# Kernel optimization log

Measured on AMD Instinct MI355X. Metric: run time of the kernel, lower is better.

## Reference

```python
import jax, jax.numpy as jnp
import numpy as np

B, L, D = 8, 30, 512
NS, NI = 21, 8  # n_slot_caps = n_slots+1, n_intent_caps = n_intents+1


def setup_inputs() -> dict:
    key = jax.random.key(0)
    ks = jax.random.split(key, 6)
    s = 0.02  # keep pose magnitudes sane
    return {
        "token_features": jax.random.normal(ks[0], (B, L, D), jnp.float32),
        "cls_token": jax.random.normal(ks[1], (B, D), jnp.float32),
        "w_route_ws": jax.random.normal(ks[2], (L, NS, D), jnp.float32) * s,
        "w_pose_ws": jax.random.normal(ks[3], (L, NS, D, D), jnp.float32) * s,
        "w_route_si": jax.random.normal(ks[4], (NS, NI, D), jnp.float32) * s,
        "w_pose_si": jax.random.normal(ks[5], (NS, NI, D, D), jnp.float32) * s,
    }


def reference(token_features, cls_token, w_route_ws, w_pose_ws, w_route_si, w_pose_si):
    d_model = token_features.shape[-1]
    # ---- route words -> slots ----
    a_words = token_features.sum(-1) / d_model                      # (b, l)
    c_ws = jax.nn.softmax(
        jnp.einsum('lnj,blj->bln', w_route_ws, token_features), axis=-1)  # (b, l, n_slot)
    wc = c_ws * a_words[:, :, None]                                 # (b, l, n_slot)
    weighted_c = wc.sum(axis=1)                                     # (b, n_slot)
    a_slots = weighted_c / a_words.sum(-1, keepdims=True)           # (b, n_slot)
    u_hat_slots = jnp.einsum('lnij,blj->blni', w_pose_ws, token_features)  # (b, l, n_slot, d)
    u_slots = jnp.einsum('bls,blsk->bsk', wc, u_hat_slots) / weighted_c[:, :, None]
    slots = jnp.argmax(c_ws, axis=-1)                               # (b, l)
    # ---- route slots -> intents ----
    c_si = jax.nn.softmax(
        jnp.einsum('sij,bsj->bsi', w_route_si, u_slots), axis=-1)   # (b, n_slot, n_int)
    wc2 = c_si * a_slots[:, :, None]                                # (b, n_slot, n_int)
    weighted_c2 = wc2.sum(axis=1)                                   # (b, n_int)
    a_intents = weighted_c2 / a_slots.sum(-1, keepdims=True)        # (b, n_int)
    u_hat_intents = jnp.einsum('sijk,bsk->bsik', w_pose_si, u_slots)  # (b, n_slot, n_int, d)
    u_intents = jnp.einsum('bsi,bsik->bik', wc2, u_hat_intents) / weighted_c2[:, :, None]
    # ---- argmax dispatch + cls residual ----
    max_idx = jnp.argmax(a_intents, axis=-1)                        # (b,)
    poses = jnp.take_along_axis(u_intents, max_idx[:, None, None], axis=1)[:, 0, :]
    intents = cls_token + poses                                     # (b, d)
    return (slots, intents)
```

## Files before the change

### kernel.cpp

```cpp
#include <hip/hip_runtime.h>

#define B 8
#define L 30
#define D 512
#define NS 21
#define NI 8

__device__ __forceinline__ float block_reduce_sum_256(float v, float* red) {
  int lane = threadIdx.x & 63;
  int wid  = threadIdx.x >> 6;
  #pragma unroll
  for (int o = 32; o > 0; o >>= 1) v += __shfl_down(v, o, 64);
  __syncthreads();
  if (lane == 0) red[wid] = v;
  __syncthreads();
  float r = 0.f;
  if (threadIdx.x == 0) {
    #pragma unroll
    for (int w = 0; w < 4; w++) r += red[w];
  }
  return r;
}

__global__ void k_phase_a(const float* __restrict__ x,
                          const float* __restrict__ w_route_ws,
                          float* __restrict__ wc,
                          float* __restrict__ a_words,
                          float* __restrict__ slots_out) {
  __shared__ float red[4];
  __shared__ float logits[NS];
  __shared__ float s_aw;
  int bl = blockIdx.x;
  int l  = bl % L;
  const float* xv = x + (size_t)bl * D;

  float p = 0.f;
  for (int j = threadIdx.x; j < D; j += 256) p += xv[j];
  float tot = block_reduce_sum_256(p, red);
  if (threadIdx.x == 0) { s_aw = tot / (float)D; a_words[bl] = s_aw; }

  for (int n = 0; n < NS; n++) {
    const float* wr = w_route_ws + (size_t)(l * NS + n) * D;
    float q = 0.f;
    for (int j = threadIdx.x; j < D; j += 256) q += wr[j] * xv[j];
    float t = block_reduce_sum_256(q, red);
    if (threadIdx.x == 0) logits[n] = t;
  }
  __syncthreads();
  if (threadIdx.x == 0) {
    float m = logits[0]; int am = 0;
    #pragma unroll
    for (int n = 1; n < NS; n++) if (logits[n] > m) { m = logits[n]; am = n; }
    float e[NS]; float se = 0.f;
    #pragma unroll
    for (int n = 0; n < NS; n++) { e[n] = __expf(logits[n] - m); se += e[n]; }
    float sc = s_aw / se;
    #pragma unroll
    for (int n = 0; n < NS; n++) wc[(size_t)bl * NS + n] = e[n] * sc;
    slots_out[bl] = (float)am;
  }
}

__global__ void k_stats1(const float* __restrict__ wc,
                         const float* __restrict__ a_words,
                         float* __restrict__ weighted_c,
                         float* __restrict__ a_slots) {
  __shared__ float aw_sum[B];
  int t = threadIdx.x;
  if (t < B) {
    float s = 0.f;
    for (int l = 0; l < L; l++) s += a_words[t * L + l];
    aw_sum[t] = s;
  }
  __syncthreads();
  if (t < B * NS) {
    int b = t / NS, n = t % NS;
    float s = 0.f;
    for (int l = 0; l < L; l++) s += wc[(size_t)(b * L + l) * NS + n];
    weighted_c[t] = s;
    a_slots[t] = s / aw_sum[b];
  }
}

__global__ void __launch_bounds__(256) k_u_slots(
    const float* __restrict__ x,
    const float* __restrict__ w_pose_ws,
    const float* __restrict__ wc,
    const float* __restrict__ weighted_c,
    float* __restrict__ u_slots) {
  __shared__ float lwc[B * L];
  __shared__ float lwcn[B];
  int n     = blockIdx.x >> 5;
  int itile = blockIdx.x & 31;
  int wave  = threadIdx.x >> 6;
  int lane  = threadIdx.x & 63;
  int i0    = itile * 16 + wave * 4;

  if (threadIdx.x < B * L) lwc[threadIdx.x] = wc[(size_t)threadIdx.x * NS + n];
  if (threadIdx.x >= 240 && threadIdx.x < 240 + B)
    lwcn[threadIdx.x - 240] = weighted_c[(threadIdx.x - 240) * NS + n];
  __syncthreads();

  float acc[4][B];
  #pragma unroll
  for (int r = 0; r < 4; r++)
    #pragma unroll
    for (int b = 0; b < B; b++) acc[r][b] = 0.f;

  for (int l = 0; l < L; l++) {
    const float* wrow = w_pose_ws + ((size_t)(l * NS + n) * D + i0) * D;
    float4 w0[4], w1[4];
    #pragma unroll
    for (int r = 0; r < 4; r++) {
      const float4* wp = (const float4*)(wrow + (size_t)r * D) + lane * 2;
      w0[r] = wp[0]; w1[r] = wp[1];
    }
    #pragma unroll
    for (int b = 0; b < B; b++) {
      const float4* xp = (const float4*)(x + (size_t)(b * L + l) * D) + lane * 2;
      float4 x0 = xp[0], x1 = xp[1];
      float wcl = lwc[b * L + l];
      #pragma unroll
      for (int r = 0; r < 4; r++) {
        float t = w0[r].x * x0.x + w0[r].y * x0.y + w0[r].z * x0.z + w0[r].w * x0.w
                + w1[r].x * x1.x + w1[r].y * x1.y + w1[r].z * x1.z + w1[r].w * x1.w;
        acc[r][b] += wcl * t;
      }
    }
  }
  #pragma unroll
  for (int r = 0; r < 4; r++)
    #pragma unroll
    for (int b = 0; b < B; b++)
      #pragma unroll
      for (int o = 32; o > 0; o >>= 1) acc[r][b] += __shfl_xor(acc[r][b], o, 64);
  if (lane == 0) {
    #pragma unroll
    for (int r = 0; r < 4; r++)
      #pragma unroll
      for (int b = 0; b < B; b++)
        u_slots[((size_t)b * NS + n) * D + (i0 + r)] = acc[r][b] / lwcn[b];
  }
}

__global__ void k_route_si(const float* __restrict__ u_slots,
                           const float* __restrict__ w_route_si,
                           const float* __restrict__ a_slots,
                           float* __restrict__ wc2) {
  __shared__ float red[4];
  __shared__ float logits[NI];
  int bs = blockIdx.x;
  int s  = bs % NS;
  const float* uv = u_slots + (size_t)bs * D;
  for (int i = 0; i < NI; i++) {
    const float* wr = w_route_si + (size_t)(s * NI + i) * D;
    float q = 0.f;
    for (int j = threadIdx.x; j < D; j += 256) q += wr[j] * uv[j];
    float t = block_reduce_sum_256(q, red);
    if (threadIdx.x == 0) logits[i] = t;
  }
  __syncthreads();
  if (threadIdx.x == 0) {
    float m = logits[0];
    #pragma unroll
    for (int i = 1; i < NI; i++) m = fmaxf(m, logits[i]);
    float e[NI]; float se = 0.f;
    #pragma unroll
    for (int i = 0; i < NI; i++) { e[i] = __expf(logits[i] - m); se += e[i]; }
    float sc = a_slots[bs] / se;
    #pragma unroll
    for (int i = 0; i < NI; i++) wc2[(size_t)bs * NI + i] = e[i] * sc;
  }
}

__global__ void k_stats2(const float* __restrict__ wc2,
                         const float* __restrict__ a_slots,
                         float* __restrict__ weighted_c2,
                         int* __restrict__ max_idx) {
  __shared__ float asum[B];
  __shared__ float ai[B * NI];
  int t = threadIdx.x;
  if (t < B) {
    float s = 0.f;
    for (int n = 0; n < NS; n++) s += a_slots[t * NS + n];
    asum[t] = s;
  }
  float w = 0.f;
  if (t < B * NI) {
    int b = t / NI, i = t % NI;
    for (int ss = 0; ss < NS; ss++) w += wc2[(size_t)(b * NS + ss) * NI + i];
    weighted_c2[t] = w;
  }
  __syncthreads();
  if (t < B * NI) ai[t] = w / asum[t / NI];
  __syncthreads();
  if (t < B) {
    float m = ai[t * NI]; int am = 0;
    #pragma unroll
    for (int i = 1; i < NI; i++) { float v = ai[t * NI + i]; if (v > m) { m = v; am = i; } }
    max_idx[t] = am;
  }
}

__global__ void k_pose_si(const float* __restrict__ w_pose_si,
                          const float* __restrict__ u_slots,
                          const float* __restrict__ wc2,
                          const int* __restrict__ max_idx,
                          float* __restrict__ poses) {
  const int JS = 4;
  int idx = blockIdx.x;
  int b   = idx / (NS * JS);
  int rem = idx - b * (NS * JS);
  int s   = rem / JS, jc = rem % JS;
  int i   = max_idx[b];
  int k   = threadIdx.x;
  const float* wb = w_pose_si + (size_t)(s * NI + i) * D * D + k;
  float cs = 0.f;
  int j0 = jc * (D / JS);
  #pragma unroll 8
  for (int j = j0; j < j0 + D / JS; j++) cs += wb[(size_t)j * D];
  float val = wc2[(size_t)(b * NS + s) * NI + i] *
              u_slots[(size_t)(b * NS + s) * D + k] * cs;
  atomicAdd(&poses[b * D + k], val);
}

__global__ void k_final(const float* __restrict__ cls,
                        const float* __restrict__ poses,
                        const float* __restrict__ weighted_c2,
                        const int* __restrict__ max_idx,
                        float* __restrict__ out_intents) {
  int b = blockIdx.x, k = threadIdx.x;
  out_intents[b * D + k] =
      cls[b * D + k] + poses[b * D + k] / weighted_c2[b * NI + max_idx[b]];
}

extern "C" void kernel_launch(void* const* d_in, const int* in_sizes, int n_in,
                              void* d_out, int out_size, void* d_ws, size_t ws_size,
                              hipStream_t stream) {
  const float* x    = (const float*)d_in[0];
  const float* cls  = (const float*)d_in[1];
  const float* wrws = (const float*)d_in[2];
  const float* wpws = (const float*)d_in[3];
  const float* wrsi = (const float*)d_in[4];
  const float* wpsi = (const float*)d_in[5];

  float* out         = (float*)d_out;
  float* slots_out   = out;
  float* intents_out = out + B * L;

  float* wsf         = (float*)d_ws;
  float* wc          = wsf;
  float* a_words     = wc + B * L * NS;
  float* weighted_c  = a_words + B * L;
  float* a_slots     = weighted_c + B * NS;
  float* u_slots     = a_slots + B * NS;
  float* wc2         = u_slots + B * NS * D;
  float* weighted_c2 = wc2 + B * NS * NI;
  float* poses       = weighted_c2 + B * NI;
  int*   max_idx     = (int*)(poses + B * D);

  hipMemsetAsync(poses, 0, B * D * sizeof(float), stream);
  k_phase_a<<<B * L, 256, 0, stream>>>(x, wrws, wc, a_words, slots_out);
  k_stats1<<<1, 256, 0, stream>>>(wc, a_words, weighted_c, a_slots);
  k_u_slots<<<NS * 32, 256, 0, stream>>>(x, wpws, wc, weighted_c, u_slots);
  k_route_si<<<B * NS, 256, 0, stream>>>(u_slots, wrsi, a_slots, wc2);
  k_stats2<<<1, 256, 0, stream>>>(wc2, a_slots, weighted_c2, max_idx);
  k_pose_si<<<B * NS * 4, 512, 0, stream>>>(wpsi, u_slots, wc2, max_idx, poses);
  k_final<<<B, 512, 0, stream>>>(cls, poses, weighted_c2, max_idx, intents_out);
}
```

Baseline: 1.036 ms.

## Split u_slots over L chunks, dedupe pose_si column sums, wave-level routing dots

```diff
diff --git a/kernel.cpp b/kernel.cpp
--- a/kernel.cpp
+++ b/kernel.cpp
@@ -5,48 +5,44 @@
 #define D 512
 #define NS 21
 #define NI 8
-
-__device__ __forceinline__ float block_reduce_sum_256(float v, float* red) {
+#define LC 5
+#define LPC (L / LC)
+
+__global__ void __launch_bounds__(256) k_phase_a(
+    const float* __restrict__ x,
+    const float* __restrict__ w_route_ws,
+    float* __restrict__ wc,
+    float* __restrict__ a_words,
+    float* __restrict__ slots_out) {
+  __shared__ float logits[NS];
+  int bl   = blockIdx.x;
+  int l    = bl % L;
+  int wave = threadIdx.x >> 6;
   int lane = threadIdx.x & 63;
-  int wid  = threadIdx.x >> 6;
-  #pragma unroll
-  for (int o = 32; o > 0; o >>= 1) v += __shfl_down(v, o, 64);
-  __syncthreads();
-  if (lane == 0) red[wid] = v;
-  __syncthreads();
-  float r = 0.f;
-  if (threadIdx.x == 0) {
-    #pragma unroll
-    for (int w = 0; w < 4; w++) r += red[w];
-  }
-  return r;
-}
-
-__global__ void k_phase_a(const float* __restrict__ x,
-                          const float* __restrict__ w_route_ws,
-                          float* __restrict__ wc,
-                          float* __restrict__ a_words,
-                          float* __restrict__ slots_out) {
-  __shared__ float red[4];
-  __shared__ float logits[NS];
-  __shared__ float s_aw;
-  int bl = blockIdx.x;
-  int l  = bl % L;
-  const float* xv = x + (size_t)bl * D;
-
-  float p = 0.f;
-  for (int j = threadIdx.x; j < D; j += 256) p += xv[j];
-  float tot = block_reduce_sum_256(p, red);
-  if (threadIdx.x == 0) { s_aw = tot / (float)D; a_words[bl] = s_aw; }
-
-  for (int n = 0; n < NS; n++) {
-    const float* wr = w_route_ws + (size_t)(l * NS + n) * D;
-    float q = 0.f;
-    for (int j = threadIdx.x; j < D; j += 256) q += wr[j] * xv[j];
-    float t = block_reduce_sum_256(q, red);
-    if (threadIdx.x == 0) logits[n] = t;
-  }
-  __syncthreads();
+
+  const float4* xp = (const float4*)(x + (size_t)bl * D) + lane * 2;
+  float4 x0 = xp[0], x1 = xp[1];
+
+  float aw = 0.f;
+  if (wave == 0) {
+    float s = x0.x + x0.y + x0.z + x0.w + x1.x + x1.y + x1.z + x1.w;
+    #pragma unroll
+    for (int o = 32; o > 0; o >>= 1) s += __shfl_xor(s, o, 64);
+    aw = s / (float)D;
+    if (lane == 0) a_words[bl] = aw;
+  }
+
+  for (int n = wave; n < NS; n += 4) {
+    const float4* wp = (const float4*)(w_route_ws + (size_t)(l * NS + n) * D) + lane * 2;
+    float4 w0 = wp[0], w1 = wp[1];
+    float q = w0.x * x0.x + w0.y * x0.y + w0.z * x0.z + w0.w * x0.w
+            + w1.x * x1.x + w1.y * x1.y + w1.z * x1.z + w1.w * x1.w;
+    #pragma unroll
+    for (int o = 32; o > 0; o >>= 1) q += __shfl_xor(q, o, 64);
+    if (lane == 0) logits[n] = q;
+  }
+  __syncthreads();
+
   if (threadIdx.x == 0) {
     float m = logits[0]; int am = 0;
     #pragma unroll
@@ -54,7 +50,7 @@
     float e[NS]; float se = 0.f;
     #pragma unroll
     for (int n = 0; n < NS; n++) { e[n] = __expf(logits[n] - m); se += e[n]; }
-    float sc = s_aw / se;
+    float sc = aw / se;
     #pragma unroll
     for (int n = 0; n < NS; n++) wc[(size_t)bl * NS + n] = e[n] * sc;
     slots_out[bl] = (float)am;
@@ -86,19 +82,18 @@
     const float* __restrict__ x,
     const float* __restrict__ w_pose_ws,
     const float* __restrict__ wc,
-    const float* __restrict__ weighted_c,
-    float* __restrict__ u_slots) {
+    float* __restrict__ u_part) {
   __shared__ float lwc[B * L];
-  __shared__ float lwcn[B];
-  int n     = blockIdx.x >> 5;
-  int itile = blockIdx.x & 31;
+  int bid   = blockIdx.x;
+  int n     = bid / (32 * LC);
+  int rem   = bid % (32 * LC);
+  int itile = rem / LC;
+  int lc    = rem % LC;
   int wave  = threadIdx.x >> 6;
   int lane  = threadIdx.x & 63;
   int i0    = itile * 16 + wave * 4;
 
   if (threadIdx.x < B * L) lwc[threadIdx.x] = wc[(size_t)threadIdx.x * NS + n];
-  if (threadIdx.x >= 240 && threadIdx.x < 240 + B)
-    lwcn[threadIdx.x - 240] = weighted_c[(threadIdx.x - 240) * NS + n];
   __syncthreads();
 
   float acc[4][B];
@@ -107,7 +102,8 @@
     #pragma unroll
     for (int b = 0; b < B; b++) acc[r][b] = 0.f;
 
-  for (int l = 0; l < L; l++) {
+  int l0 = lc * LPC;
+  for (int l = l0; l < l0 + LPC; l++) {
     const float* wrow = w_pose_ws + ((size_t)(l * NS + n) * D + i0) * D;
     float4 w0[4], w1[4];
     #pragma unroll
@@ -139,25 +135,47 @@
     for (int r = 0; r < 4; r++)
       #pragma unroll
       for (int b = 0; b < B; b++)
-        u_slots[((size_t)b * NS + n) * D + (i0 + r)] = acc[r][b] / lwcn[b];
-  }
-}
-
-__global__ void k_route_si(const float* __restrict__ u_slots,
-                           const float* __restrict__ w_route_si,
-                           const float* __restrict__ a_slots,
-                           float* __restrict__ wc2) {
-  __shared__ float red[4];
+        u_part[(((size_t)lc * B + b) * NS + n) * D + (i0 + r)] = acc[r][b];
+  }
+}
+
+__global__ void k_div_u(const float* __restrict__ u_part,
+                        const float* __restrict__ weighted_c,
+                        float* __restrict__ u_slots) {
+  int bn = blockIdx.x;
+  int b  = bn / NS, n = bn % NS;
+  float wcn = weighted_c[bn];
+  for (int k = threadIdx.x; k < D; k += 256) {
+    float s = 0.f;
+    #pragma unroll
+    for (int lc = 0; lc < LC; lc++)
+      s += u_part[(((size_t)lc * B + b) * NS + n) * D + k];
+    u_slots[(size_t)bn * D + k] = s / wcn;
+  }
+}
+
+__global__ void __launch_bounds__(256) k_route_si(
+    const float* __restrict__ u_slots,
+    const float* __restrict__ w_route_si,
+    const float* __restrict__ a_slots,
+    float* __restrict__ wc2) {
   __shared__ float logits[NI];
-  int bs = blockIdx.x;
-  int s  = bs % NS;
-  const float* uv = u_slots + (size_t)bs * D;
-  for (int i = 0; i < NI; i++) {
-    const float* wr = w_route_si + (size_t)(s * NI + i) * D;
-    float q = 0.f;
-    for (int j = threadIdx.x; j < D; j += 256) q += wr[j] * uv[j];
-    float t = block_reduce_sum_256(q, red);
-    if (threadIdx.x == 0) logits[i] = t;
+  int bs   = blockIdx.x;
+  int s    = bs % NS;
+  int wave = threadIdx.x >> 6;
+  int lane = threadIdx.x & 63;
+
+  const float4* up = (const float4*)(u_slots + (size_t)bs * D) + lane * 2;
+  float4 u0 = up[0], u1 = up[1];
+
+  for (int i = wave; i < NI; i += 4) {
+    const float4* wp = (const float4*)(w_route_si + (size_t)(s * NI + i) * D) + lane * 2;
+    float4 w0 = wp[0], w1 = wp[1];
+    float q = w0.x * u0.x + w0.y * u0.y + w0.z * u0.z + w0.w * u0.w
+            + w1.x * u1.x + w1.y * u1.y + w1.z * u1.z + w1.w * u1.w;
+    #pragma unroll
+    for (int o = 32; o > 0; o >>= 1) q += __shfl_xor(q, o, 64);
+    if (lane == 0) logits[i] = q;
   }
   __syncthreads();
   if (threadIdx.x == 0) {
@@ -202,36 +220,59 @@
   }
 }
 
-__global__ void k_pose_si(const float* __restrict__ w_pose_si,
-                          const float* __restrict__ u_slots,
-                          const float* __restrict__ wc2,
-                          const int* __restrict__ max_idx,
-                          float* __restrict__ poses) {
-  const int JS = 4;
-  int idx = blockIdx.x;
-  int b   = idx / (NS * JS);
-  int rem = idx - b * (NS * JS);
-  int s   = rem / JS, jc = rem % JS;
-  int i   = max_idx[b];
-  int k   = threadIdx.x;
-  const float* wb = w_pose_si + (size_t)(s * NI + i) * D * D + k;
-  float cs = 0.f;
-  int j0 = jc * (D / JS);
-  #pragma unroll 8
-  for (int j = j0; j < j0 + D / JS; j++) cs += wb[(size_t)j * D];
-  float val = wc2[(size_t)(b * NS + s) * NI + i] *
-              u_slots[(size_t)(b * NS + s) * D + k] * cs;
-  atomicAdd(&poses[b * D + k], val);
-}
-
-__global__ void k_final(const float* __restrict__ cls,
-                        const float* __restrict__ poses,
-                        const float* __restrict__ weighted_c2,
-                        const int* __restrict__ max_idx,
-                        float* __restrict__ out_intents) {
+__global__ void __launch_bounds__(256) k_colsum(
+    const float* __restrict__ w_pose_si,
+    const int* __restrict__ max_idx,
+    float* __restrict__ colsum_part) {
+  int blk = blockIdx.x;
+  int si  = blk >> 2;
+  int i   = si & (NI - 1);
+  int jc  = blk & 3;
+  bool sel = false;
+  #pragma unroll
+  for (int b = 0; b < B; b++) sel |= (max_idx[b] == i);
+  if (!sel) return;
+
+  int t  = threadIdx.x;
+  int k4 = t & 127;
+  int jg = t >> 7;
+  const float4* wb = (const float4*)(w_pose_si + (size_t)si * D * D) + k4;
+  int j0 = jc * 128 + jg * 64;
+  float4 s = {0.f, 0.f, 0.f, 0.f};
+  #pragma unroll 4
+  for (int j = j0; j < j0 + 64; j++) {
+    float4 v = wb[(size_t)j * (D / 4)];
+    s.x += v.x; s.y += v.y; s.z += v.z; s.w += v.w;
+  }
+  __shared__ float4 part[128];
+  if (jg == 0) part[k4] = s;
+  __syncthreads();
+  if (jg == 1) {
+    float4 p = part[k4];
+    p.x += s.x; p.y += s.y; p.z += s.z; p.w += s.w;
+    ((float4*)colsum_part)[(size_t)(jc * NS * NI + si) * (D / 4) + k4] = p;
+  }
+}
+
+__global__ void k_final2(const float* __restrict__ cls,
+                         const float* __restrict__ u_slots,
+                         const float* __restrict__ wc2,
+                         const float* __restrict__ weighted_c2,
+                         const int* __restrict__ max_idx,
+                         const float* __restrict__ colsum_part,
+                         float* __restrict__ out_intents) {
   int b = blockIdx.x, k = threadIdx.x;
-  out_intents[b * D + k] =
-      cls[b * D + k] + poses[b * D + k] / weighted_c2[b * NI + max_idx[b]];
+  int i = max_idx[b];
+  float acc = 0.f;
+  for (int s = 0; s < NS; s++) {
+    float cs = 0.f;
+    #pragma unroll
+    for (int jc = 0; jc < 4; jc++)
+      cs += colsum_part[(size_t)(jc * NS * NI + s * NI + i) * D + k];
+    acc += wc2[(size_t)(b * NS + s) * NI + i] *
+           u_slots[(size_t)(b * NS + s) * D + k] * cs;
+  }
+  out_intents[b * D + k] = cls[b * D + k] + acc / weighted_c2[b * NI + i];
 }
 
 extern "C" void kernel_launch(void* const* d_in, const int* in_sizes, int n_in,
@@ -254,17 +295,19 @@
   float* weighted_c  = a_words + B * L;
   float* a_slots     = weighted_c + B * NS;
   float* u_slots     = a_slots + B * NS;
-  float* wc2         = u_slots + B * NS * D;
+  float* u_part      = u_slots + B * NS * D;
+  float* wc2         = u_part + LC * B * NS * D;
   float* weighted_c2 = wc2 + B * NS * NI;
-  float* poses       = weighted_c2 + B * NI;
-  int*   max_idx     = (int*)(poses + B * D);
-
-  hipMemsetAsync(poses, 0, B * D * sizeof(float), stream);
+  int*   max_idx     = (int*)(weighted_c2 + B * NI);
+  float* colsum_part = (float*)(max_idx + 8);
+
   k_phase_a<<<B * L, 256, 0, stream>>>(x, wrws, wc, a_words, slots_out);
   k_stats1<<<1, 256, 0, stream>>>(wc, a_words, weighted_c, a_slots);
-  k_u_slots<<<NS * 32, 256, 0, stream>>>(x, wpws, wc, weighted_c, u_slots);
+  k_u_slots<<<NS * 32 * LC, 256, 0, stream>>>(x, wpws, wc, u_part);
+  k_div_u<<<B * NS, 256, 0, stream>>>(u_part, weighted_c, u_slots);
   k_route_si<<<B * NS, 256, 0, stream>>>(u_slots, wrsi, a_slots, wc2);
   k_stats2<<<1, 256, 0, stream>>>(wc2, a_slots, weighted_c2, max_idx);
-  k_pose_si<<<B * NS * 4, 512, 0, stream>>>(wpsi, u_slots, wc2, max_idx, poses);
-  k_final<<<B, 512, 0, stream>>>(cls, poses, weighted_c2, max_idx, intents_out);
-}
+  k_colsum<<<NS * NI * 4, 256, 0, stream>>>(wpsi, max_idx, colsum_part);
+  k_final2<<<B, 512, 0, stream>>>(cls, u_slots, wc2, weighted_c2, max_idx,
+                                  colsum_part, intents_out);
+}
```

Result: faster. 1.003 ms (-3.1%).
